# Performance work log

Measured on AMD Instinct MI355X. Metric: run time of the kernel, lower is better.

The kernel has to match this reference:

```python
import jax, jax.numpy as jnp
import numpy as np

D_MODEL = 2048
EXPAND = 2
D_INNER = EXPAND * D_MODEL          # 4096 == d_ssm
D_STATE = 128
NGROUPS = 1
HEADDIM = 64
NHEADS = D_INNER // HEADDIM          # 64
D_CONV = 4
CHUNK = 128
D_XBC = D_INNER + 2 * NGROUPS * D_STATE   # 4352
D_IN_PROJ = 2 * D_INNER + 2 * NGROUPS * D_STATE + NHEADS  # 8512
EPS = 1e-5


def setup_inputs() -> dict:
    key = jax.random.key(0)
    ks = jax.random.split(key, 9)
    u = jax.random.normal(ks[0], (2, 2048, D_MODEL), dtype=jnp.float32)
    W_in = jax.random.normal(ks[1], (D_IN_PROJ, D_MODEL), dtype=jnp.float32) / np.sqrt(D_MODEL)
    conv_w = jax.random.normal(ks[2], (D_XBC, D_CONV), dtype=jnp.float32) / np.sqrt(D_CONV)
    conv_b = jax.random.normal(ks[3], (D_XBC,), dtype=jnp.float32) * 0.1
    dt_bias = jnp.log(jnp.expm1(jax.random.uniform(ks[4], (NHEADS,), minval=0.001, maxval=0.1)))
    A_log = jnp.log(jax.random.uniform(ks[5], (NHEADS,), minval=1.0, maxval=16.0))
    D = jnp.ones((NHEADS,), dtype=jnp.float32)
    norm_weight = jnp.ones((D_INNER,), dtype=jnp.float32)
    W_out = jax.random.normal(ks[8], (D_MODEL, D_INNER), dtype=jnp.float32) / np.sqrt(D_INNER)
    return {"u": u, "W_in": W_in, "conv_w": conv_w, "conv_b": conv_b,
            "dt_bias": dt_bias, "A_log": A_log, "D": D,
            "norm_weight": norm_weight, "W_out": W_out}


def _causal_conv1d(xBC, conv_w, conv_b):
    # xBC: [b, l, d]; depthwise causal conv of width D_CONV, then SiLU
    x = jnp.transpose(xBC, (0, 2, 1))                      # [b, d, l]
    x = jnp.pad(x, ((0, 0), (0, 0), (D_CONV - 1, 0)))
    y = jax.lax.conv_general_dilated(
        x, conv_w[:, None, :], window_strides=(1,), padding='VALID',
        feature_group_count=D_XBC, dimension_numbers=('NCH', 'OIH', 'NCH'))
    y = y + conv_b[None, :, None]
    return jnp.transpose(jax.nn.silu(y), (0, 2, 1))        # [b, l, d]


def _ssd(x, dt, A, B, C, D):
    # x: [b,l,h,p]; dt: [b,l,h] (post-softplus); A: [h]; B,C: [b,l,g,n]; D: [h]
    b, L, h, p = x.shape
    n = B.shape[-1]
    c = L // CHUNK
    hpg = h // NGROUPS
    Bh = jnp.repeat(B, hpg, axis=2)                        # [b,l,h,n]
    Ch = jnp.repeat(C, hpg, axis=2)
    xr = x.reshape(b, c, CHUNK, h, p)
    dtr = dt.reshape(b, c, CHUNK, h)
    Br = Bh.reshape(b, c, CHUNK, h, n)
    Cr = Ch.reshape(b, c, CHUNK, h, n)
    xdt = xr * dtr[..., None]                              # [b,c,l,h,p]
    dA = jnp.transpose((dt * A[None, None, :]).reshape(b, c, CHUNK, h), (0, 3, 1, 2))  # [b,h,c,l]
    A_cs = jnp.cumsum(dA, axis=-1)                         # [b,h,c,l]
    # intra-chunk decay matrix L[i,j] = exp(sum_{j+1..i} dA), lower-triangular
    diff = A_cs[..., :, None] - A_cs[..., None, :]         # [b,h,c,l,s]
    mask = jnp.tril(jnp.ones((CHUNK, CHUNK), dtype=bool))
    Lmat = jnp.where(mask, jnp.exp(jnp.where(mask, diff, 0.0)), 0.0)
    Y_diag = jnp.einsum('bclhn,bcshn,bhcls,bcshp->bclhp', Cr, Br, Lmat, xdt)
    decay_states = jnp.exp(A_cs[..., -1:] - A_cs)          # [b,h,c,l]
    states = jnp.einsum('bclhn,bhcl,bclhp->bchpn', Br, decay_states, xdt)
    chunk_decay = jnp.exp(A_cs[..., -1])                   # [b,h,c]
    # inter-chunk recurrence over c chunks
    def step(carry, inp):
        s, d = inp                                         # s:[b,h,p,n], d:[b,h]
        return carry * d[..., None, None] + s, carry
    init = jnp.zeros((b, h, p, n), dtype=x.dtype)
    _, prev = jax.lax.scan(step, init,
                           (jnp.transpose(states, (1, 0, 2, 3, 4)),
                            jnp.transpose(chunk_decay, (2, 0, 1))))
    prev_states = jnp.transpose(prev, (1, 0, 2, 3, 4))     # [b,c,h,p,n]
    Y_off = jnp.einsum('bclhn,bchpn,bhcl->bclhp', Cr, prev_states, jnp.exp(A_cs))
    Y = (Y_diag + Y_off).reshape(b, L, h, p) + x * D[None, None, :, None]
    return Y


def reference(u, W_in, conv_w, conv_b, dt_bias, A_log, D, norm_weight, W_out):
    b, L, _ = u.shape
    zxbcdt = jnp.einsum('bld,ed->ble', u, W_in)            # [b,l,8512]
    z = zxbcdt[..., :D_INNER]
    xBC = zxbcdt[..., D_INNER:D_INNER + D_XBC]
    dt = zxbcdt[..., D_INNER + D_XBC:]                     # [b,l,h]
    xBC = _causal_conv1d(xBC, conv_w, conv_b)
    x = xBC[..., :D_INNER]
    B = xBC[..., D_INNER:D_INNER + NGROUPS * D_STATE].reshape(b, L, NGROUPS, D_STATE)
    C = xBC[..., D_INNER + NGROUPS * D_STATE:].reshape(b, L, NGROUPS, D_STATE)
    dt = jax.nn.softplus(dt + dt_bias[None, None, :])
    A = -jnp.exp(A_log)
    y = _ssd(x.reshape(b, L, NHEADS, HEADDIM), dt, A, B, C, D)
    y = y.reshape(b, L, D_INNER)
    # gated RMSNorm (norm_before_gate=False): norm(y * silu(z))
    yg = y * jax.nn.silu(z)
    y = yg * jax.lax.rsqrt(jnp.mean(yg * yg, axis=-1, keepdims=True) + EPS) * norm_weight
    return jnp.einsum('bld,ed->ble', y, W_out)
```

## Files before the change

### kernel.cpp

```cpp
#include <hip/hip_runtime.h>
#include <cstdint>
#include <cstddef>

#define SEQ     2048
#define NBATCH  2
#define BL      (NBATCH*SEQ)
#define DMODEL  2048
#define DINNER  4096
#define DSTATE  128
#define HEADDIM 64
#define NHEADS  64
#define DXBC    4352
#define DPROJ   8512
#define NPAD    8576
#define NCHUNK  16
#define CHUNKL  128

typedef __bf16 bf16x8_t __attribute__((ext_vector_type(8)));
typedef float f32x4_t __attribute__((ext_vector_type(4)));
typedef unsigned short u16x8_t __attribute__((ext_vector_type(8)));
typedef unsigned short u16x4_t __attribute__((ext_vector_type(4)));
typedef __attribute__((address_space(1))) unsigned int as1_u32;
typedef __attribute__((address_space(3))) unsigned int as3_u32;

__device__ __forceinline__ unsigned short f2bf(float f) {
  unsigned u = __builtin_bit_cast(unsigned, f);
  u += 0x7FFFu + ((u >> 16) & 1u);
  return (unsigned short)(u >> 16);
}
__device__ __forceinline__ float bf2f(unsigned short h) {
  unsigned u = ((unsigned)h) << 16;
  return __builtin_bit_cast(float, u);
}
__device__ __forceinline__ void gload16(const void* g, void* l) {
  __builtin_amdgcn_global_load_lds((const as1_u32*)g, (as3_u32*)l, 16, 0, 0);
}
__device__ __forceinline__ f32x4_t mfma16(u16x8_t a, u16x8_t b, f32x4_t c) {
  return __builtin_amdgcn_mfma_f32_16x16x32_bf16(
      __builtin_bit_cast(bf16x8_t, a), __builtin_bit_cast(bf16x8_t, b), c, 0, 0, 0);
}
__device__ __forceinline__ float siluf(float x) { return x / (1.f + __expf(-x)); }

__global__ __launch_bounds__(256) void cvt_kernel(const float* __restrict__ src,
                                                  unsigned short* __restrict__ dst, int n) {
  int idx = (blockIdx.x * 256 + threadIdx.x) * 4;
  if (idx >= n) return;
  float4 v = *(const float4*)&src[idx];
  u16x4_t o; o[0] = f2bf(v.x); o[1] = f2bf(v.y); o[2] = f2bf(v.z); o[3] = f2bf(v.w);
  *(u16x4_t*)&dst[idx] = o;
}

__global__ __launch_bounds__(256) void cvt_win_kernel(const float* __restrict__ W,
                                                      unsigned short* __restrict__ dst) {
  int idx = (blockIdx.x * 256 + threadIdx.x) * 4;
  if (idx >= NPAD * DMODEL) return;
  int e = idx / DMODEL;
  u16x4_t o;
  if (e < DPROJ) {
    float4 v = *(const float4*)&W[idx];
    o[0] = f2bf(v.x); o[1] = f2bf(v.y); o[2] = f2bf(v.z); o[3] = f2bf(v.w);
  } else {
    o[0] = 0; o[1] = 0; o[2] = 0; o[3] = 0;
  }
  *(u16x4_t*)&dst[idx] = o;
}

template <bool BF16OUT>
__global__ __launch_bounds__(256) void gemm_bt_kernel(const unsigned short* __restrict__ A,
                                                      const unsigned short* __restrict__ B,
                                                      void* __restrict__ Cp,
                                                      int M, int N, int K) {
  __shared__ unsigned short As[128 * 64];
  __shared__ unsigned short Bs[128 * 64];
  const int n0 = blockIdx.x * 128;
  const int m0 = blockIdx.y * 128;
  const int t = threadIdx.x, lane = t & 63, w = t >> 6;
  const int wr = w >> 1, wc = w & 1;
  const int srow = t >> 3;
  const int scol = (t & 7) * 8;
  f32x4_t acc[4][4];
#pragma unroll
  for (int i = 0; i < 4; ++i)
#pragma unroll
    for (int j = 0; j < 4; ++j) acc[i][j] = (f32x4_t){0.f, 0.f, 0.f, 0.f};

  const int nk = K >> 6;
  for (int kt = 0; kt < nk; ++kt) {
    const int k0 = kt << 6;
#pragma unroll
    for (int s = 0; s < 4; ++s) {
      int r = s * 32 + srow;
      gload16(&A[(size_t)(m0 + r) * K + k0 + scol], &As[r * 64 + scol]);
      gload16(&B[(size_t)(n0 + r) * K + k0 + scol], &Bs[r * 64 + scol]);
    }
    __syncthreads();
#pragma unroll
    for (int ks = 0; ks < 2; ++ks) {
      const int kk = ks * 32 + (lane >> 4) * 8;
      u16x8_t af[4], bfr[4];
#pragma unroll
      for (int i = 0; i < 4; ++i) {
        af[i]  = *(const u16x8_t*)&As[(wr * 64 + i * 16 + (lane & 15)) * 64 + kk];
        bfr[i] = *(const u16x8_t*)&Bs[(wc * 64 + i * 16 + (lane & 15)) * 64 + kk];
      }
#pragma unroll
      for (int i = 0; i < 4; ++i)
#pragma unroll
        for (int j = 0; j < 4; ++j) acc[i][j] = mfma16(af[i], bfr[j], acc[i][j]);
    }
    __syncthreads();
  }
#pragma unroll
  for (int i = 0; i < 4; ++i) {
    const int mbase = m0 + wr * 64 + i * 16 + (lane >> 4) * 4;
#pragma unroll
    for (int j = 0; j < 4; ++j) {
      const int n = n0 + wc * 64 + j * 16 + (lane & 15);
#pragma unroll
      for (int r = 0; r < 4; ++r) {
        if (BF16OUT) ((unsigned short*)Cp)[(size_t)(mbase + r) * N + n] = f2bf(acc[i][j][r]);
        else         ((float*)Cp)[(size_t)(mbase + r) * N + n] = acc[i][j][r];
      }
    }
  }
}

__global__ __launch_bounds__(256) void conv_kernel(const unsigned short* __restrict__ zx,
                                                   const float* __restrict__ conv_w,
                                                   const float* __restrict__ conv_b,
                                                   unsigned short* __restrict__ xc) {
  long long idx = (long long)blockIdx.x * 256 + threadIdx.x;
  if (idx >= (long long)BL * DXBC) return;
  int e = (int)(idx % DXBC);
  int bl = (int)(idx / DXBC);
  int l = bl % SEQ, b = bl / SEQ;
  float acc = conv_b[e];
#pragma unroll
  for (int wi = 0; wi < 4; ++wi) {
    int ll = l - 3 + wi;
    if (ll >= 0) acc += bf2f(zx[((size_t)b * SEQ + ll) * NPAD + DINNER + e]) * conv_w[e * 4 + wi];
  }
  xc[(size_t)bl * DXBC + e] = f2bf(siluf(acc));
}

__global__ __launch_bounds__(128) void dt_kernel(const unsigned short* __restrict__ zx,
                                                 const float* __restrict__ dt_bias,
                                                 const float* __restrict__ A_log,
                                                 float* __restrict__ dt_soft,
                                                 float* __restrict__ Acs,
                                                 float* __restrict__ cdecay) {
  int blk = blockIdx.x;
  int c = blk & 15, h = (blk >> 4) & 63, b = blk >> 10;
  int i = threadIdx.x;
  int l = c * CHUNKL + i;
  float raw = bf2f(zx[((size_t)b * SEQ + l) * NPAD + (DINNER + DXBC) + h]) + dt_bias[h];
  float dt = (raw > 20.f) ? raw : log1pf(__expf(raw));
  dt_soft[((size_t)b * 64 + h) * SEQ + l] = dt;
  float A = -__expf(A_log[h]);
  __shared__ float sbuf[128];
  sbuf[i] = dt * A;
  __syncthreads();
  for (int ofs = 1; ofs < 128; ofs <<= 1) {
    float v = (i >= ofs) ? sbuf[i - ofs] : 0.f;
    __syncthreads();
    sbuf[i] += v;
    __syncthreads();
  }
  float cs = sbuf[i];
  Acs[(((size_t)b * 64 + h) * 16 + c) * 128 + i] = cs;
  if (i == 127) cdecay[((size_t)b * 64 + h) * 16 + c] = __expf(cs);
}

__global__ __launch_bounds__(256) void xdt_kernel(const unsigned short* __restrict__ xc,
                                                  const float* __restrict__ dt_soft,
                                                  unsigned short* __restrict__ xdtT) {
  int blk = blockIdx.x;
  int lt = blk & 15, h = (blk >> 4) & 63, b = blk >> 10;
  __shared__ unsigned short tile[128][66];
  __shared__ float dts[128];
  int t = threadIdx.x;
  const unsigned short* xg = xc + ((size_t)b * SEQ + lt * 128) * DXBC + h * 64;
#pragma unroll
  for (int k = 0; k < 32; ++k) {
    int idx = t + k * 256;
    int row = idx >> 6, col = idx & 63;
    tile[row][col] = xg[(size_t)row * DXBC + col];
  }
  if (t < 128) dts[t] = dt_soft[((size_t)b * 64 + h) * SEQ + lt * 128 + t];
  __syncthreads();
  unsigned short* xo = xdtT + (((size_t)b * 64 + h) * 64) * SEQ + lt * 128;
#pragma unroll
  for (int k = 0; k < 32; ++k) {
    int idx = t + k * 256;
    int p = idx >> 7, j = idx & 127;
    xo[(size_t)p * SEQ + j] = f2bf(bf2f(tile[j][p]) * dts[j]);
  }
}

__global__ __launch_bounds__(256) void btr_kernel(const unsigned short* __restrict__ xc,
                                                  unsigned short* __restrict__ BT) {
  int blk = blockIdx.x;
  int lt = blk & 15, b = blk >> 4;
  __shared__ unsigned short tile[128][129];
  int t = threadIdx.x;
  const unsigned short* src = xc + ((size_t)b * SEQ + lt * 128) * DXBC + DINNER;
#pragma unroll
  for (int k = 0; k < 64; ++k) {
    int idx = t + k * 256;
    int j = idx >> 7, n = idx & 127;
    tile[j][n] = src[(size_t)j * DXBC + n];
  }
  __syncthreads();
  unsigned short* dst = BT + (size_t)b * 128 * SEQ + lt * 128;
#pragma unroll
  for (int k = 0; k < 64; ++k) {
    int idx = t + k * 256;
    int n = idx >> 7, j = idx & 127;
    dst[(size_t)n * SEQ + j] = tile[j][n];
  }
}

__global__ __launch_bounds__(256) void ssd_states_kernel(const unsigned short* __restrict__ BT,
                                                         const unsigned short* __restrict__ xdtT,
                                                         const float* __restrict__ Acs,
                                                         float* __restrict__ states) {
  int blk = blockIdx.x;
  int h = blk & 63, c = (blk >> 6) & 15, b = blk >> 10;
  __shared__ unsigned short BTs[128 * 128];
  __shared__ unsigned short xs[64 * 128];
  __shared__ float dec[128];
  int t = threadIdx.x, lane = t & 63, w = t >> 6, wr = w >> 1, wc = w & 1;
  int srow = t >> 4, scol = (t & 15) * 8;
  const unsigned short* BTb = BT + (size_t)b * 128 * SEQ + c * 128;
#pragma unroll
  for (int s = 0; s < 8; ++s) {
    int r = s * 16 + srow;
    gload16(&BTb[(size_t)r * SEQ + scol], &BTs[r * 128 + scol]);
  }
  const unsigned short* xb = xdtT + (((size_t)b * 64 + h) * 64) * SEQ + c * 128;
#pragma unroll
  for (int s = 0; s < 4; ++s) {
    int r = s * 16 + srow;
    gload16(&xb[(size_t)r * SEQ + scol], &xs[r * 128 + scol]);
  }
  const float* acsr = Acs + (((size_t)b * 64 + h) * 16 + c) * 128;
  float alast = acsr[127];
  if (t < 128) dec[t] = __expf(alast - acsr[t]);
  __syncthreads();

  f32x4_t acc[2][4];
#pragma unroll
  for (int i = 0; i < 2; ++i)
#pragma unroll
    for (int j = 0; j < 4; ++j) acc[i][j] = (f32x4_t){0.f, 0.f, 0.f, 0.f};
#pragma unroll
  for (int ks = 0; ks < 4; ++ks) {
    const int kk = ks * 32 + (lane >> 4) * 8;
    float d8[8];
#pragma unroll
    for (int e = 0; e < 8; ++e) d8[e] = dec[kk + e];
    u16x8_t af[2], bfr[4];
#pragma unroll
    for (int i = 0; i < 2; ++i) {
      u16x8_t raw = *(const u16x8_t*)&xs[(wr * 32 + i * 16 + (lane & 15)) * 128 + kk];
      u16x8_t sc;
#pragma unroll
      for (int e = 0; e < 8; ++e) sc[e] = f2bf(bf2f(raw[e]) * d8[e]);
      af[i] = sc;
    }
#pragma unroll
    for (int j = 0; j < 4; ++j)
      bfr[j] = *(const u16x8_t*)&BTs[(wc * 64 + j * 16 + (lane & 15)) * 128 + kk];
#pragma unroll
    for (int i = 0; i < 2; ++i)
#pragma unroll
      for (int j = 0; j < 4; ++j) acc[i][j] = mfma16(af[i], bfr[j], acc[i][j]);
  }
  float* so = states + ((((size_t)b * 16 + c) * 64 + h) * 64) * 128;
#pragma unroll
  for (int i = 0; i < 2; ++i) {
    int pbase = wr * 32 + i * 16 + (lane >> 4) * 4;
#pragma unroll
    for (int j = 0; j < 4; ++j) {
      int n = wc * 64 + j * 16 + (lane & 15);
#pragma unroll
      for (int r = 0; r < 4; ++r) so[(size_t)(pbase + r) * 128 + n] = acc[i][j][r];
    }
  }
}

__global__ __launch_bounds__(256) void ssd_scan_kernel(const float* __restrict__ states,
                                                       const float* __restrict__ cdecay,
                                                       unsigned short* __restrict__ prevb) {
  int blk = blockIdx.x;
  int h = blk & 63, b = blk >> 6;
  int t = threadIdx.x;
  float carry[32];
#pragma unroll
  for (int k = 0; k < 32; ++k) carry[k] = 0.f;
  const float* cd = cdecay + ((size_t)b * 64 + h) * 16;
  for (int c = 0; c < 16; ++c) {
    const float* sp = states + ((((size_t)b * 16 + c) * 64 + h) * 64) * 128;
    unsigned short* pp = prevb + ((((size_t)b * 16 + c) * 64 + h) * 64) * 128;
    float d = cd[c];
#pragma unroll
    for (int k = 0; k < 32; ++k) {
      int idx = t + k * 256;
      pp[idx] = f2bf(carry[k]);
      carry[k] = carry[k] * d + sp[idx];
    }
  }
}

__global__ __launch_bounds__(256) void ssd_y_kernel(const unsigned short* __restrict__ xc,
                                                    const unsigned short* __restrict__ xdtT,
                                                    const unsigned short* __restrict__ prevb,
                                                    const float* __restrict__ Acs,
                                                    const float* __restrict__ Dp,
                                                    float* __restrict__ Y) {
  int blk = blockIdx.x;
  int h = blk & 63, c = (blk >> 6) & 15, b = blk >> 10;
  __shared__ unsigned short Bs[128 * 128];
  __shared__ unsigned short Cs[128 * 128];
  __shared__ unsigned short xs[64 * 128];
  __shared__ unsigned short ps[64 * 128];
  __shared__ float acs_s[128];
  int t = threadIdx.x, lane = t & 63, w = t >> 6, wr = w >> 1, wc = w & 1;
  int srow = t >> 4, scol = (t & 15) * 8;
  const unsigned short* Bg = xc + ((size_t)b * SEQ + c * 128) * DXBC + DINNER;
  const unsigned short* Cg = Bg + DSTATE;
#pragma unroll
  for (int s = 0; s < 8; ++s) {
    int r = s * 16 + srow;
    gload16(&Bg[(size_t)r * DXBC + scol], &Bs[r * 128 + scol]);
    gload16(&Cg[(size_t)r * DXBC + scol], &Cs[r * 128 + scol]);
  }
  const unsigned short* xg = xdtT + (((size_t)b * 64 + h) * 64) * SEQ + c * 128;
#pragma unroll
  for (int s = 0; s < 4; ++s) {
    int r = s * 16 + srow;
    gload16(&xg[(size_t)r * SEQ + scol], &xs[r * 128 + scol]);
  }
  const unsigned short* pg = prevb + ((((size_t)b * 16 + c) * 64 + h) * 64) * 128;
#pragma unroll
  for (int s = 0; s < 4; ++s) {
    int r = s * 16 + srow;
    gload16(&pg[r * 128 + scol], &ps[r * 128 + scol]);
  }
  const float* acsr = Acs + (((size_t)b * 64 + h) * 16 + c) * 128;
  if (t < 128) acs_s[t] = acsr[t];
  __syncthreads();

  f32x4_t cbt[4][4];
#pragma unroll
  for (int i = 0; i < 4; ++i)
#pragma unroll
    for (int j = 0; j < 4; ++j) cbt[i][j] = (f32x4_t){0.f, 0.f, 0.f, 0.f};
#pragma unroll
  for (int ks = 0; ks < 4; ++ks) {
    const int kk = ks * 32 + (lane >> 4) * 8;
    u16x8_t af[4], bfr[4];
#pragma unroll
    for (int i = 0; i < 4; ++i) {
      af[i]  = *(const u16x8_t*)&Bs[(wr * 64 + i * 16 + (lane & 15)) * 128 + kk];
      bfr[i] = *(const u16x8_t*)&Cs[(wc * 64 + i * 16 + (lane & 15)) * 128 + kk];
    }
#pragma unroll
    for (int i = 0; i < 4; ++i)
#pragma unroll
      for (int j = 0; j < 4; ++j) cbt[i][j] = mfma16(af[i], bfr[j], cbt[i][j]);
  }
  __syncthreads();
#pragma unroll
  for (int fi = 0; fi < 4; ++fi) {
#pragma unroll
    for (int fj = 0; fj < 4; ++fj) {
      int i = wc * 64 + fj * 16 + (lane & 15);
      int jb = wr * 64 + fi * 16 + (lane >> 4) * 4;
      float ai = acs_s[i];
      u16x4_t m4;
#pragma unroll
      for (int r = 0; r < 4; ++r) {
        int j = jb + r;
        float v = (i >= j) ? cbt[fi][fj][r] * __expf(ai - acs_s[j]) : 0.f;
        m4[r] = f2bf(v);
      }
      *(u16x4_t*)&Bs[i * 128 + jb] = m4;
    }
  }
  __syncthreads();

  f32x4_t accY[4][2], accO[4][2];
#pragma unroll
  for (int i = 0; i < 4; ++i)
#pragma unroll
    for (int j = 0; j < 2; ++j) {
      accY[i][j] = (f32x4_t){0.f, 0.f, 0.f, 0.f};
      accO[i][j] = (f32x4_t){0.f, 0.f, 0.f, 0.f};
    }
#pragma unroll
  for (int ks = 0; ks < 4; ++ks) {
    const int kk = ks * 32 + (lane >> 4) * 8;
    u16x8_t af[4], bfr[2], cf[4], pf[2];
#pragma unroll
    for (int i = 0; i < 4; ++i) {
      af[i] = *(const u16x8_t*)&Bs[(wr * 64 + i * 16 + (lane & 15)) * 128 + kk];
      cf[i] = *(const u16x8_t*)&Cs[(wr * 64 + i * 16 + (lane & 15)) * 128 + kk];
    }
#pragma unroll
    for (int j = 0; j < 2; ++j) {
      bfr[j] = *(const u16x8_t*)&xs[(wc * 32 + j * 16 + (lane & 15)) * 128 + kk];
      pf[j]  = *(const u16x8_t*)&ps[(wc * 32 + j * 16 + (lane & 15)) * 128 + kk];
    }
#pragma unroll
    for (int i = 0; i < 4; ++i)
#pragma unroll
      for (int j = 0; j < 2; ++j) {
        accY[i][j] = mfma16(af[i], bfr[j], accY[i][j]);
        accO[i][j] = mfma16(cf[i], pf[j], accO[i][j]);
      }
  }
  float Dh = Dp[h];
  float* Yo = Y + ((size_t)b * SEQ + c * 128) * DINNER + h * 64;
  const unsigned short* xo = xc + ((size_t)b * SEQ + c * 128) * DXBC + h * 64;
#pragma unroll
  for (int fi = 0; fi < 4; ++fi) {
    int ibase = wr * 64 + fi * 16 + (lane >> 4) * 4;
#pragma unroll
    for (int r = 0; r < 4; ++r) {
      int i = ibase + r;
      float esc = __expf(acs_s[i]);
#pragma unroll
      for (int fj = 0; fj < 2; ++fj) {
        int p = wc * 32 + fj * 16 + (lane & 15);
        float v = accY[fi][fj][r] + accO[fi][fj][r] * esc + bf2f(xo[(size_t)i * DXBC + p]) * Dh;
        Yo[(size_t)i * DINNER + p] = v;
      }
    }
  }
}

__global__ __launch_bounds__(256) void norm_kernel(const float* __restrict__ Y,
                                                   const unsigned short* __restrict__ zx,
                                                   const float* __restrict__ nw,
                                                   unsigned short* __restrict__ yn) {
  int bl = blockIdx.x;
  const float* yr = Y + (size_t)bl * DINNER;
  const unsigned short* zr = zx + (size_t)bl * NPAD;
  int t = threadIdx.x;
  float vals[16];
  float ss = 0.f;
#pragma unroll
  for (int k = 0; k < 16; ++k) {
    int d = t + k * 256;
    float g = yr[d] * siluf(bf2f(zr[d]));
    vals[k] = g;
    ss += g * g;
  }
#pragma unroll
  for (int o = 32; o > 0; o >>= 1) ss += __shfl_down(ss, o, 64);
  __shared__ float red[4];
  if ((t & 63) == 0) red[t >> 6] = ss;
  __syncthreads();
  float tot = red[0] + red[1] + red[2] + red[3];
  float rs = rsqrtf(tot * (1.f / (float)DINNER) + 1e-5f);
#pragma unroll
  for (int k = 0; k < 16; ++k) {
    int d = t + k * 256;
    yn[(size_t)bl * DINNER + d] = f2bf(vals[k] * rs * nw[d]);
  }
}

extern "C" void kernel_launch(void* const* d_in, const int* in_sizes, int n_in,
                              void* d_out, int out_size, void* d_ws, size_t ws_size,
                              hipStream_t stream) {
  const float* u       = (const float*)d_in[0];
  const float* W_in    = (const float*)d_in[1];
  const float* conv_w  = (const float*)d_in[2];
  const float* conv_b  = (const float*)d_in[3];
  const float* dt_bias = (const float*)d_in[4];
  const float* A_log   = (const float*)d_in[5];
  const float* Dv      = (const float*)d_in[6];
  const float* norm_w  = (const float*)d_in[7];
  const float* W_out   = (const float*)d_in[8];
  float* out = (float*)d_out;
  (void)in_sizes; (void)n_in; (void)out_size;

  const size_t SZ_UBF    = (size_t)BL * DMODEL * 2;
  const size_t SZ_WIN    = (size_t)NPAD * DMODEL * 2;
  const size_t SZ_WOUT   = (size_t)DMODEL * DINNER * 2;
  const size_t SZ_XDTT   = (size_t)NBATCH * NHEADS * HEADDIM * SEQ * 2;
  const size_t SZ_ZX     = (size_t)BL * NPAD * 2;
  const size_t SZ_XC     = (size_t)BL * DXBC * 2;
  const size_t SZ_BT     = (size_t)NBATCH * DSTATE * SEQ * 2;
  const size_t SZ_DTS    = (size_t)NBATCH * NHEADS * SEQ * 4;
  const size_t SZ_ACS    = (size_t)NBATCH * NHEADS * NCHUNK * 128 * 4;
  const size_t SZ_CDEC   = (size_t)NBATCH * NHEADS * NCHUNK * 4;
  const size_t SZ_STATES = (size_t)NBATCH * NCHUNK * NHEADS * HEADDIM * DSTATE * 4;
  const size_t SZ_PREV   = (size_t)NBATCH * NCHUNK * NHEADS * HEADDIM * DSTATE * 2;
  const size_t REGION_A  = SZ_UBF + SZ_WIN;

  char* ws = (char*)d_ws;
  size_t off = 0;
  auto alloc = [&](size_t bytes) { char* p = ws + off; off += (bytes + 255) & ~(size_t)255; return p; };

  char* regionA = alloc(REGION_A);
  unsigned short* zx     = (unsigned short*)alloc(SZ_ZX);
  unsigned short* xc     = (unsigned short*)alloc(SZ_XC);
  unsigned short* BT     = (unsigned short*)alloc(SZ_BT);
  float* dt_soft         = (float*)alloc(SZ_DTS);
  float* Acs             = (float*)alloc(SZ_ACS);
  float* cdecay          = (float*)alloc(SZ_CDEC);
  char* statesYb         = alloc(SZ_STATES);
  char* prevYn           = alloc(SZ_PREV);
  if (off > ws_size) return;

  unsigned short* u_bf    = (unsigned short*)regionA;
  unsigned short* win_bf  = (unsigned short*)(regionA + SZ_UBF);
  unsigned short* xdtT    = (unsigned short*)regionA;
  unsigned short* wout_bf = (unsigned short*)(regionA + SZ_XDTT);
  float* states           = (float*)statesYb;
  float* Yb               = (float*)statesYb;
  unsigned short* prevb   = (unsigned short*)prevYn;
  unsigned short* yn      = (unsigned short*)prevYn;

  cvt_kernel<<<dim3((BL * DMODEL / 4 + 255) / 256), dim3(256), 0, stream>>>(u, u_bf, BL * DMODEL);
  cvt_win_kernel<<<dim3(NPAD * DMODEL / 4 / 256), dim3(256), 0, stream>>>(W_in, win_bf);

  gemm_bt_kernel<true><<<dim3(NPAD / 128, BL / 128), dim3(256), 0, stream>>>(u_bf, win_bf, zx, BL, NPAD, DMODEL);

  cvt_kernel<<<dim3((DMODEL * DINNER / 4 + 255) / 256), dim3(256), 0, stream>>>(W_out, wout_bf, DMODEL * DINNER);

  conv_kernel<<<dim3((int)(((size_t)BL * DXBC + 255) / 256)), dim3(256), 0, stream>>>(zx, conv_w, conv_b, xc);

  dt_kernel<<<dim3(NBATCH * NHEADS * NCHUNK), dim3(128), 0, stream>>>(zx, dt_bias, A_log, dt_soft, Acs, cdecay);

  xdt_kernel<<<dim3(NBATCH * NHEADS * NCHUNK), dim3(256), 0, stream>>>(xc, dt_soft, xdtT);
  btr_kernel<<<dim3(NBATCH * (SEQ / 128)), dim3(256), 0, stream>>>(xc, BT);

  ssd_states_kernel<<<dim3(NBATCH * NCHUNK * NHEADS), dim3(256), 0, stream>>>(BT, xdtT, Acs, states);
  ssd_scan_kernel<<<dim3(NBATCH * NHEADS), dim3(256), 0, stream>>>(states, cdecay, prevb);
  ssd_y_kernel<<<dim3(NBATCH * NCHUNK * NHEADS), dim3(256), 0, stream>>>(xc, xdtT, prevb, Acs, Dv, Yb);

  norm_kernel<<<dim3(BL), dim3(256), 0, stream>>>(Yb, zx, norm_w, yn);

  gemm_bt_kernel<false><<<dim3(DMODEL / 128, BL / 128), dim3(256), 0, stream>>>(yn, wout_bf, out, BL, DMODEL, DINNER);
}
```

Before: 634.5 us.

## Remap GEMM tiles for XCD/L2 locality, split scan wider, store Y as bf16

Both GEMMs move to a 1D grid with an XCD-aware block remap: blocks are interleaved across the 8 dies, then grouped in bands of 4 M-tiles so that neighbouring tiles share L2. The SSD scan kernel splits each (batch, head) over 8 blocks, which gives 8x more blocks and fewer registers per thread. The SSD output Y is now written as bf16 instead of fp32, which halves traffic between ssd_y and norm at some cost in precision. The remap assumes the grid size divides evenly by 8 and the band layout.

```diff
diff --git a/kernel.cpp b/kernel.cpp
--- a/kernel.cpp
+++ b/kernel.cpp
@@ -69,11 +69,19 @@
 __global__ __launch_bounds__(256) void gemm_bt_kernel(const unsigned short* __restrict__ A,
                                                       const unsigned short* __restrict__ B,
                                                       void* __restrict__ Cp,
-                                                      int M, int N, int K) {
+                                                      int M, int N, int K, int gx) {
   __shared__ unsigned short As[128 * 64];
   __shared__ unsigned short Bs[128 * 64];
-  const int n0 = blockIdx.x * 128;
-  const int m0 = blockIdx.y * 128;
+  const int nwg = gridDim.x;
+  const int q = nwg >> 3;
+  const int l = blockIdx.x;
+  const int newid = (l & 7) * q + (l >> 3);
+  const int band = newid / (gx * 4);
+  const int idx  = newid % (gx * 4);
+  const int bn = idx >> 2;
+  const int bm = band * 4 + (idx & 3);
+  const int n0 = bn * 128;
+  const int m0 = bm * 128;
   const int t = threadIdx.x, lane = t & 63, w = t >> 6;
   const int wr = w >> 1, wc = w & 1;
   const int srow = t >> 3;
@@ -293,23 +301,23 @@
                                                        const float* __restrict__ cdecay,
                                                        unsigned short* __restrict__ prevb) {
   int blk = blockIdx.x;
-  int h = blk & 63, b = blk >> 6;
+  int s = blk & 7, h = (blk >> 3) & 63, b = blk >> 9;
   int t = threadIdx.x;
-  float carry[32];
-#pragma unroll
-  for (int k = 0; k < 32; ++k) carry[k] = 0.f;
+  float carry[4] = {0.f, 0.f, 0.f, 0.f};
   const float* cd = cdecay + ((size_t)b * 64 + h) * 16;
+  const size_t hoff = ((size_t)b * 16) * 64 + h;
   for (int c = 0; c < 16; ++c) {
-    const float* sp = states + ((((size_t)b * 16 + c) * 64 + h) * 64) * 128;
-    unsigned short* pp = prevb + ((((size_t)b * 16 + c) * 64 + h) * 64) * 128;
+    const float* sp = states + (((size_t)(b * 16 + c) * 64 + h) * 64) * 128;
+    unsigned short* pp = prevb + (((size_t)(b * 16 + c) * 64 + h) * 64) * 128;
     float d = cd[c];
 #pragma unroll
-    for (int k = 0; k < 32; ++k) {
-      int idx = t + k * 256;
-      pp[idx] = f2bf(carry[k]);
-      carry[k] = carry[k] * d + sp[idx];
-    }
-  }
+    for (int k = 0; k < 4; ++k) {
+      int e = s * 1024 + k * 256 + t;
+      pp[e] = f2bf(carry[k]);
+      carry[k] = carry[k] * d + sp[e];
+    }
+  }
+  (void)hoff;
 }
 
 __global__ __launch_bounds__(256) void ssd_y_kernel(const unsigned short* __restrict__ xc,
@@ -317,7 +325,7 @@
                                                     const unsigned short* __restrict__ prevb,
                                                     const float* __restrict__ Acs,
                                                     const float* __restrict__ Dp,
-                                                    float* __restrict__ Y) {
+                                                    unsigned short* __restrict__ Y) {
   int blk = blockIdx.x;
   int h = blk & 63, c = (blk >> 6) & 15, b = blk >> 10;
   __shared__ unsigned short Bs[128 * 128];
@@ -421,7 +429,7 @@
       }
   }
   float Dh = Dp[h];
-  float* Yo = Y + ((size_t)b * SEQ + c * 128) * DINNER + h * 64;
+  unsigned short* Yo = Y + ((size_t)b * SEQ + c * 128) * DINNER + h * 64;
   const unsigned short* xo = xc + ((size_t)b * SEQ + c * 128) * DXBC + h * 64;
 #pragma unroll
   for (int fi = 0; fi < 4; ++fi) {
@@ -434,18 +442,18 @@
       for (int fj = 0; fj < 2; ++fj) {
         int p = wc * 32 + fj * 16 + (lane & 15);
         float v = accY[fi][fj][r] + accO[fi][fj][r] * esc + bf2f(xo[(size_t)i * DXBC + p]) * Dh;
-        Yo[(size_t)i * DINNER + p] = v;
+        Yo[(size_t)i * DINNER + p] = f2bf(v);
       }
     }
   }
 }
 
-__global__ __launch_bounds__(256) void norm_kernel(const float* __restrict__ Y,
+__global__ __launch_bounds__(256) void norm_kernel(const unsigned short* __restrict__ Y,
                                                    const unsigned short* __restrict__ zx,
                                                    const float* __restrict__ nw,
                                                    unsigned short* __restrict__ yn) {
   int bl = blockIdx.x;
-  const float* yr = Y + (size_t)bl * DINNER;
+  const unsigned short* yr = Y + (size_t)bl * DINNER;
   const unsigned short* zr = zx + (size_t)bl * NPAD;
   int t = threadIdx.x;
   float vals[16];
@@ -453,7 +461,7 @@
 #pragma unroll
   for (int k = 0; k < 16; ++k) {
     int d = t + k * 256;
-    float g = yr[d] * siluf(bf2f(zr[d]));
+    float g = bf2f(yr[d]) * siluf(bf2f(zr[d]));
     vals[k] = g;
     ss += g * g;
   }
@@ -488,7 +496,6 @@
 
   const size_t SZ_UBF    = (size_t)BL * DMODEL * 2;
   const size_t SZ_WIN    = (size_t)NPAD * DMODEL * 2;
-  const size_t SZ_WOUT   = (size_t)DMODEL * DINNER * 2;
   const size_t SZ_XDTT   = (size_t)NBATCH * NHEADS * HEADDIM * SEQ * 2;
   const size_t SZ_ZX     = (size_t)BL * NPAD * 2;
   const size_t SZ_XC     = (size_t)BL * DXBC * 2;
@@ -520,14 +527,15 @@
   unsigned short* xdtT    = (unsigned short*)regionA;
   unsigned short* wout_bf = (unsigned short*)(regionA + SZ_XDTT);
   float* states           = (float*)statesYb;
-  float* Yb               = (float*)statesYb;
+  unsigned short* Yb      = (unsigned short*)statesYb;
   unsigned short* prevb   = (unsigned short*)prevYn;
   unsigned short* yn      = (unsigned short*)prevYn;
 
   cvt_kernel<<<dim3((BL * DMODEL / 4 + 255) / 256), dim3(256), 0, stream>>>(u, u_bf, BL * DMODEL);
   cvt_win_kernel<<<dim3(NPAD * DMODEL / 4 / 256), dim3(256), 0, stream>>>(W_in, win_bf);
 
-  gemm_bt_kernel<true><<<dim3(NPAD / 128, BL / 128), dim3(256), 0, stream>>>(u_bf, win_bf, zx, BL, NPAD, DMODEL);
+  gemm_bt_kernel<true><<<dim3((NPAD / 128) * (BL / 128)), dim3(256), 0, stream>>>(
+      u_bf, win_bf, zx, BL, NPAD, DMODEL, NPAD / 128);
 
   cvt_kernel<<<dim3((DMODEL * DINNER / 4 + 255) / 256), dim3(256), 0, stream>>>(W_out, wout_bf, DMODEL * DINNER);
 
@@ -539,10 +547,11 @@
   btr_kernel<<<dim3(NBATCH * (SEQ / 128)), dim3(256), 0, stream>>>(xc, BT);
 
   ssd_states_kernel<<<dim3(NBATCH * NCHUNK * NHEADS), dim3(256), 0, stream>>>(BT, xdtT, Acs, states);
-  ssd_scan_kernel<<<dim3(NBATCH * NHEADS), dim3(256), 0, stream>>>(states, cdecay, prevb);
+  ssd_scan_kernel<<<dim3(NBATCH * NHEADS * 8), dim3(256), 0, stream>>>(states, cdecay, prevb);
   ssd_y_kernel<<<dim3(NBATCH * NCHUNK * NHEADS), dim3(256), 0, stream>>>(xc, xdtT, prevb, Acs, Dv, Yb);
 
   norm_kernel<<<dim3(BL), dim3(256), 0, stream>>>(Yb, zx, norm_w, yn);
 
-  gemm_bt_kernel<false><<<dim3(DMODEL / 128, BL / 128), dim3(256), 0, stream>>>(yn, wout_bf, out, BL, DMODEL, DINNER);
-}
+  gemm_bt_kernel<false><<<dim3((DMODEL / 128) * (BL / 128)), dim3(256), 0, stream>>>(
+      yn, wout_bf, out, BL, DMODEL, DINNER, DMODEL / 128);
+}
```

New measurement: 628.6 us. No clear change (-0.9%).
